# Kernel tuning notes

Hardware: AMD Instinct MI355X
Metric: run time of the kernel (lower is better)

Reference implementation:

```python
import jax, jax.numpy as jnp
import numpy as np

N_GAUSS, FEAT = 2048, 128
H, W = 128, 128
FX, FY = 128.0, 128.0
CX, CY = W / 2.0, H / 2.0
MAX_STEP = 0.05          # xyz_offset_max_step
CLIP_SCALING = 0.2       # clip_scaling
LOW_PASS = 0.3           # 2D covariance dilation (as in reference CUDA rasterizer)


def _quat_to_rot(q):
    # q: [N,4] normalized, (w,x,y,z) convention (rotation bias init has 1 at index 0)
    w, x, y, z = q[:, 0], q[:, 1], q[:, 2], q[:, 3]
    R = jnp.stack([
        1 - 2 * (y * y + z * z), 2 * (x * y - w * z), 2 * (x * z + w * y),
        2 * (x * y + w * z), 1 - 2 * (x * x + z * z), 2 * (y * z - w * x),
        2 * (x * z - w * y), 2 * (y * z + w * x), 1 - 2 * (x * x + y * y),
    ], axis=-1)
    return R.reshape(-1, 3, 3)


def setup_inputs() -> dict:
    key = jax.random.key(0)
    ks = jax.random.split(key, 8)
    s = 0.02
    x = jax.random.normal(ks[0], (N_GAUSS, FEAT), jnp.float32)
    pts = jax.random.normal(ks[1], (N_GAUSS, 3), jnp.float32) * 0.4
    # camera 2.5 units in front of the point cloud, looking down +z (view z = z + 2.5)
    viewmat = jnp.asarray(np.array(
        [[1, 0, 0, 0], [0, 1, 0, 0], [0, 0, 1, 2.5], [0, 0, 0, 1]], dtype=np.float32))
    w_shs = jax.random.normal(ks[2], (3, FEAT), jnp.float32) * s
    b_shs = jnp.zeros((3,), jnp.float32)
    w_scale = jax.random.normal(ks[3], (3, FEAT), jnp.float32) * s
    b_scale = jnp.full((3,), -3.0, jnp.float32)              # init_scaling
    w_xyz = jax.random.normal(ks[4], (3, FEAT), jnp.float32) * s
    b_xyz = jnp.zeros((3,), jnp.float32)
    w_opac = jax.random.normal(ks[5], (1, FEAT), jnp.float32) * s
    b_opac = jnp.full((1,), -2.1972246, jnp.float32)         # inverse_sigmoid(0.1)
    w_rot = jax.random.normal(ks[6], (4, FEAT), jnp.float32) * s
    b_rot = jnp.array([1.0, 0.0, 0.0, 0.0], jnp.float32)
    return dict(x=x, pts=pts, viewmat=viewmat, w_shs=w_shs, b_shs=b_shs,
                w_scale=w_scale, b_scale=b_scale, w_xyz=w_xyz, b_xyz=b_xyz,
                w_opac=w_opac, b_opac=b_opac, w_rot=w_rot, b_rot=b_rot)


def _forward(x, pts, viewmat, w_shs, b_shs, w_scale, b_scale, w_xyz, b_xyz,
             w_opac, b_opac, w_rot, b_rot):
    # ---- GSLayer decode (use_rgb=True path) ----
    rgb = jax.nn.sigmoid(x @ w_shs.T + b_shs)                     # [N,3]
    scale = jnp.clip(jnp.exp(x @ w_scale.T + b_scale), 0.0, CLIP_SCALING)
    offset = (jax.nn.sigmoid(x @ w_xyz.T + b_xyz) - 0.5) * MAX_STEP
    xyz = pts + offset                                            # [N,3]
    opac = jax.nn.sigmoid(x @ w_opac.T + b_opac)                  # [N,1]
    q = x @ w_rot.T + b_rot
    q = q / jnp.linalg.norm(q, axis=-1, keepdims=True)
    R = _quat_to_rot(q)                                           # [N,3,3]
    cov3d = jnp.einsum('nij,nj,nkj->nik', R, scale * scale, R)    # R S^2 R^T

    # ---- projection (EWA splatting) ----
    Rv, tv = viewmat[:3, :3], viewmat[:3, 3]
    p = xyz @ Rv.T + tv                                           # view space [N,3]
    tx, ty = p[:, 0], p[:, 1]
    tz = jnp.maximum(p[:, 2], 1e-3)
    u = FX * tx / tz + CX
    v = FY * ty / tz + CY
    zr = jnp.zeros_like(tz)
    J = jnp.stack([
        jnp.stack([FX / tz, zr, -FX * tx / (tz * tz)], axis=-1),
        jnp.stack([zr, FY / tz, -FY * ty / (tz * tz)], axis=-1),
    ], axis=1)                                                    # [N,2,3]
    M = jnp.einsum('nij,jk->nik', J, Rv)                          # [N,2,3]
    C2 = jnp.einsum('nij,njk,nlk->nil', M, cov3d, M)              # [N,2,2]
    a = C2[:, 0, 0] + LOW_PASS
    b = C2[:, 0, 1]
    c = C2[:, 1, 1] + LOW_PASS
    det = a * c - b * b + 1e-12
    cA, cB, cC = c / det, -b / det, a / det                       # conic

    # ---- per-pixel gaussian eval ----
    px = jnp.arange(W, dtype=jnp.float32) + 0.5
    py = jnp.arange(H, dtype=jnp.float32) + 0.5
    gx = jnp.tile(px, H)                                          # [P]
    gy = jnp.repeat(py, W)                                        # [P]
    dx = gx[None, :] - u[:, None]                                 # [N,P]
    dy = gy[None, :] - v[:, None]
    power = -0.5 * (cA[:, None] * dx * dx + cC[:, None] * dy * dy) - cB[:, None] * dx * dy
    power = jnp.minimum(power, 0.0)
    alpha = jnp.minimum(0.99, opac * jnp.exp(power))              # [N,P]
    vis = (p[:, 2] > 0.01).astype(alpha.dtype)[:, None]           # znear cull
    alpha = alpha * vis
    alpha = jnp.where(alpha < 1.0 / 255.0, 0.0, alpha)

    # ---- depth-sorted alpha compositing ----
    order = jnp.argsort(tz)
    alpha_s = alpha[order]
    rgb_s = rgb[order]
    T = jnp.cumprod(1.0 - alpha_s, axis=0)
    T_excl = jnp.concatenate([jnp.ones_like(T[:1]), T[:-1]], axis=0)
    wgt = alpha_s * T_excl                                        # [N,P]
    img = jnp.einsum('np,nc->pc', wgt, rgb_s).reshape(H, W, 3)
    return img


def reference(x, pts, viewmat, w_shs, b_shs, w_scale, b_scale, w_xyz, b_xyz,
              w_opac, b_opac, w_rot, b_rot):
    return _forward(x, pts, viewmat, w_shs, b_shs, w_scale, b_scale,
                    w_xyz, b_xyz, w_opac, b_opac, w_rot, b_rot)
```

## Files before the change

### kernel.cpp

```cpp
#include <hip/hip_runtime.h>
#include <math.h>

#define NG 2048
#define FEATN 128
#define NBLK 256
#define LOG2E 1.4426950408889634f
#define MAGIC1 0x7F3DC0DEu
#define MAGIC2 0x6B42F00Du

typedef unsigned long long u64;

#define RB_BYTE   32768
#define RC_BYTE   65536
#define KEY_BYTE  98304
#define SORT_BYTE 131072
#define F1_BYTE   229376
#define F2_BYTE   230400

__device__ __forceinline__ float sigmoidf_(float z) { return 1.0f / (1.0f + expf(-z)); }

__device__ __forceinline__ void stg8(void* p, u64 v) {
    __hip_atomic_store((u64*)p, v, __ATOMIC_RELAXED, __HIP_MEMORY_SCOPE_AGENT);
}
__device__ __forceinline__ void stg4(unsigned* p, unsigned v) {
    __hip_atomic_store(p, v, __ATOMIC_RELAXED, __HIP_MEMORY_SCOPE_AGENT);
}
__device__ __forceinline__ unsigned ldg4(const unsigned* p) {
    return __hip_atomic_load(p, __ATOMIC_RELAXED, __HIP_MEMORY_SCOPE_AGENT);
}
__device__ __forceinline__ void st_f4(void* p, float4 v) {
    union { float2 f; u64 u; } a, b;
    a.f = make_float2(v.x, v.y); b.f = make_float2(v.z, v.w);
    stg8(p, a.u); stg8((char*)p + 8, b.u);
}

__global__ __launch_bounds__(1024) void k_fused(
    const float* __restrict__ x, const float* __restrict__ pts, const float* __restrict__ vm,
    const float* __restrict__ w_shs, const float* __restrict__ b_shs,
    const float* __restrict__ w_scale, const float* __restrict__ b_scale,
    const float* __restrict__ w_xyz, const float* __restrict__ b_xyz,
    const float* __restrict__ w_opac, const float* __restrict__ b_opac,
    const float* __restrict__ w_rot, const float* __restrict__ b_rot,
    float* __restrict__ ws, float* __restrict__ out)
{
    __shared__ __attribute__((aligned(16))) char smem_u[512 * 12 * 4];
    __shared__ unsigned short sidx16[NG];
    __shared__ float partT[16][64], partR[16][64], partG[16][64], partB[16][64];
    __shared__ int s_cnt[16];
    __shared__ int s_break;

    float* sw = (float*)smem_u;
    float (*accs)[14] = (float(*)[14])(smem_u + 7168);
    unsigned* skey32 = (unsigned*)smem_u;
    float (*params_lds)[12] = (float(*)[12])smem_u;

    const int tid = threadIdx.x;
    const int wid = tid >> 6, lane = tid & 63;
    const int bid = blockIdx.x;
    char* wsb = (char*)ws;
    unsigned* keyg = (unsigned*)(wsb + KEY_BYTE);
    unsigned* flag1 = (unsigned*)(wsb + F1_BYTE);
    unsigned* flag2 = (unsigned*)(wsb + F2_BYTE);
    u64 lmask = (1ull << lane) - 1ull;

    for (int i = tid; i < 14 * FEATN; i += 1024) {
        int r = i >> 7, c0 = i & 127;
        float v;
        if (r < 3)       v = w_shs[r * FEATN + c0];
        else if (r < 6)  v = w_scale[(r - 3) * FEATN + c0];
        else if (r < 9)  v = w_xyz[(r - 6) * FEATN + c0];
        else if (r == 9) v = w_opac[c0];
        else             v = w_rot[(r - 10) * FEATN + c0];
        sw[i] = v;
    }
    __syncthreads();
    {
        int gi = tid >> 7;
        int head = (tid >> 3) & 15;
        int sub = tid & 7;
        int g = bid * 8 + gi;
        if (head < 14) {
            const float4* xp = (const float4*)(x + (size_t)g * FEATN + sub * 16);
            const float* wp = sw + head * FEATN + sub * 16;
            float acc = 0.0f;
#pragma unroll
            for (int k4 = 0; k4 < 4; k4++) {
                float4 xv = xp[k4];
                acc += xv.x * wp[k4 * 4 + 0] + xv.y * wp[k4 * 4 + 1]
                     + xv.z * wp[k4 * 4 + 2] + xv.w * wp[k4 * 4 + 3];
            }
            acc += __shfl_xor(acc, 1);
            acc += __shfl_xor(acc, 2);
            acc += __shfl_xor(acc, 4);
            if (sub == 0) accs[gi][head] = acc;
        }
    }
    __syncthreads();
    if (tid < 8) {
        int g = bid * 8 + tid;
        float acc[14];
#pragma unroll
        for (int j = 0; j < 14; j++) acc[j] = accs[tid][j];

        float r0 = sigmoidf_(acc[0] + b_shs[0]);
        float r1 = sigmoidf_(acc[1] + b_shs[1]);
        float r2 = sigmoidf_(acc[2] + b_shs[2]);
        float s0 = fminf(expf(acc[3] + b_scale[0]), 0.2f);
        float s1 = fminf(expf(acc[4] + b_scale[1]), 0.2f);
        float s2 = fminf(expf(acc[5] + b_scale[2]), 0.2f);
        float o0 = (sigmoidf_(acc[6] + b_xyz[0]) - 0.5f) * 0.05f;
        float o1 = (sigmoidf_(acc[7] + b_xyz[1]) - 0.5f) * 0.05f;
        float o2 = (sigmoidf_(acc[8] + b_xyz[2]) - 0.5f) * 0.05f;
        float opac = sigmoidf_(acc[9] + b_opac[0]);
        float qw = acc[10] + b_rot[0];
        float qx = acc[11] + b_rot[1];
        float qy = acc[12] + b_rot[2];
        float qz = acc[13] + b_rot[3];
        float qn = sqrtf(qw * qw + qx * qx + qy * qy + qz * qz);
        qw /= qn; qx /= qn; qy /= qn; qz /= qn;

        float R[3][3];
        R[0][0] = 1.f - 2.f * (qy * qy + qz * qz);
        R[0][1] = 2.f * (qx * qy - qw * qz);
        R[0][2] = 2.f * (qx * qz + qw * qy);
        R[1][0] = 2.f * (qx * qy + qw * qz);
        R[1][1] = 1.f - 2.f * (qx * qx + qz * qz);
        R[1][2] = 2.f * (qy * qz - qw * qx);
        R[2][0] = 2.f * (qx * qz - qw * qy);
        R[2][1] = 2.f * (qy * qz + qw * qx);
        R[2][2] = 1.f - 2.f * (qx * qx + qy * qy);

        float sq[3] = { s0 * s0, s1 * s1, s2 * s2 };
        float cov[3][3];
#pragma unroll
        for (int i = 0; i < 3; i++)
#pragma unroll
            for (int k = 0; k < 3; k++)
                cov[i][k] = R[i][0] * sq[0] * R[k][0] + R[i][1] * sq[1] * R[k][1] + R[i][2] * sq[2] * R[k][2];

        float Rv[3][3], tv[3];
#pragma unroll
        for (int i = 0; i < 3; i++) {
#pragma unroll
            for (int j = 0; j < 3; j++) Rv[i][j] = vm[i * 4 + j];
            tv[i] = vm[i * 4 + 3];
        }
        float X0 = pts[g * 3 + 0] + o0;
        float X1 = pts[g * 3 + 1] + o1;
        float X2 = pts[g * 3 + 2] + o2;
        float p0 = Rv[0][0] * X0 + Rv[0][1] * X1 + Rv[0][2] * X2 + tv[0];
        float p1 = Rv[1][0] * X0 + Rv[1][1] * X1 + Rv[1][2] * X2 + tv[1];
        float p2 = Rv[2][0] * X0 + Rv[2][1] * X1 + Rv[2][2] * X2 + tv[2];
        float tz = fmaxf(p2, 0.001f);
        float u = 128.0f * p0 / tz + 64.0f;
        float v = 128.0f * p1 / tz + 64.0f;

        float j00 = 128.0f / tz, j02 = -128.0f * p0 / (tz * tz);
        float j11 = 128.0f / tz, j12 = -128.0f * p1 / (tz * tz);
        float M0[3], M1[3];
#pragma unroll
        for (int k = 0; k < 3; k++) {
            M0[k] = j00 * Rv[0][k] + j02 * Rv[2][k];
            M1[k] = j11 * Rv[1][k] + j12 * Rv[2][k];
        }
        float t0[3], t1[3];
#pragma unroll
        for (int k = 0; k < 3; k++) {
            t0[k] = M0[0] * cov[0][k] + M0[1] * cov[1][k] + M0[2] * cov[2][k];
            t1[k] = M1[0] * cov[0][k] + M1[1] * cov[1][k] + M1[2] * cov[2][k];
        }
        float A = t0[0] * M0[0] + t0[1] * M0[1] + t0[2] * M0[2] + 0.3f;
        float B = t0[0] * M1[0] + t0[1] * M1[1] + t0[2] * M1[2];
        float C = t1[0] * M1[0] + t1[1] * M1[1] + t1[2] * M1[2] + 0.3f;
        float det = A * C - B * B + 1e-12f;
        float cA = C / det, cB = -B / det, cC = A / det;

        if (p2 <= 0.01f) opac = 0.0f;

        float rx, ry;
        if (opac >= 1.0f / 255.0f) {
            float L = 2.0f * logf(255.0f * opac);
            rx = sqrtf(L * A) + 0.5f;
            ry = sqrtf(L * C) + 0.5f;
        } else {
            rx = -1e9f; ry = -1e9f;
        }

        st_f4(wsb + (size_t)g * 16,            make_float4(u, v, rx, ry));
        st_f4(wsb + RB_BYTE + (size_t)g * 16,  make_float4(-0.5f * LOG2E * cA, -LOG2E * cB, -0.5f * LOG2E * cC, opac));
        st_f4(wsb + RC_BYTE + (size_t)g * 16,  make_float4(r0, r1, r2, 0.0f));
        stg4(&keyg[g], __float_as_uint(tz));
    }

    asm volatile("s_waitcnt vmcnt(0)" ::: "memory");
    __syncthreads();
    if (tid == 0) stg4(&flag1[bid], MAGIC1);
    if (tid < 256) {
        while (ldg4(&flag1[tid]) != MAGIC1) __builtin_amdgcn_s_sleep(4);
    }
    __syncthreads();

    ((u64*)skey32)[tid] = ((const u64*)keyg)[tid];
    __syncthreads();
    if (wid < 8) {
        int g = bid * 8 + wid;
        unsigned mk = skey32[g];
        const uint4* p4 = (const uint4*)skey32;
        int cnt = 0;
#pragma unroll
        for (int q = 0; q < 8; ++q) {
            int jb = lane + (q << 6);
            uint4 kv = p4[jb];
            int j0 = jb << 2;
            cnt += (kv.x < mk || (kv.x == mk && (j0 + 0) < g)) ? 1 : 0;
            cnt += (kv.y < mk || (kv.y == mk && (j0 + 1) < g)) ? 1 : 0;
            cnt += (kv.z < mk || (kv.z == mk && (j0 + 2) < g)) ? 1 : 0;
            cnt += (kv.w < mk || (kv.w == mk && (j0 + 3) < g)) ? 1 : 0;
        }
        cnt += __shfl_xor(cnt, 1);
        cnt += __shfl_xor(cnt, 2);
        cnt += __shfl_xor(cnt, 4);
        cnt += __shfl_xor(cnt, 8);
        cnt += __shfl_xor(cnt, 16);
        cnt += __shfl_xor(cnt, 32);
        if (lane < 6) {
            const u64* src = (const u64*)(wsb + (lane >> 1) * 32768 + (size_t)g * 16 + (lane & 1) * 8);
            char* dst = wsb + SORT_BYTE + (lane >> 1) * 32768 + (size_t)cnt * 16 + (lane & 1) * 8;
            stg8(dst, *src);
        }
    }

    asm volatile("s_waitcnt vmcnt(0)" ::: "memory");
    __syncthreads();
    if (tid == 0) stg4(&flag2[bid], MAGIC2);
    if (tid < 256) {
        while (ldg4(&flag2[tid]) != MAGIC2) __builtin_amdgcn_s_sleep(4);
    }
    __syncthreads();

    const float4* SA4 = (const float4*)(wsb + SORT_BYTE);
    const float4* SB4 = (const float4*)(wsb + SORT_BYTE + 32768);
    const float4* SC4 = (const float4*)(wsb + SORT_BYTE + 65536);
    int tx0 = (bid & 15) << 3, ty0 = (bid >> 4) << 3;
    float x0 = tx0 + 0.5f, x1 = tx0 + 7.5f;
    float y0 = ty0 + 0.5f, y1 = ty0 + 7.5f;

    int n = 0;
#pragma unroll
    for (int r = 0; r < 2; ++r) {
        int s = r * 1024 + tid;
        float4 a = SA4[s];
        bool keep = (a.x + a.z >= x0) && (a.x - a.z <= x1) &&
                    (a.y + a.w >= y0) && (a.y - a.w <= y1);
        u64 m = __ballot(keep);
        if (lane == 0) s_cnt[wid] = __popcll(m);
        __syncthreads();
        int base = n, total = 0;
#pragma unroll
        for (int w = 0; w < 16; w++) {
            if (w < wid) base += s_cnt[w];
            total += s_cnt[w];
        }
        if (keep) sidx16[base + __popcll(m & lmask)] = (unsigned short)s;
        n += total;
        __syncthreads();
    }

    float gx = x0 + (float)(lane & 7);
    float gy = y0 + (float)(lane >> 3);
    float crT = 1.0f, crR = 0.0f, crG = 0.0f, crB = 0.0f;
    for (int c0 = 0; c0 < n; c0 += 512) {
        int m = min(512, n - c0);
        if (tid < m) {
            int s = sidx16[c0 + tid];
            float4 a = SA4[s];
            float4 b = SB4[s];
            float4 c = SC4[s];
            float* e = params_lds[tid];
            ((float4*)e)[0] = make_float4(a.x, a.y, b.x, b.y);
            ((float4*)e)[1] = make_float4(b.z, b.w, c.x, c.y);
            e[8] = c.z;
        }
        __syncthreads();

        int seg = (m + 15) >> 4;
        int sb = wid * seg;
        int se = min(m, sb + seg);
        float T = 1.0f, oR = 0.0f, oG = 0.0f, oB = 0.0f;
        for (int i = sb; i < se; ++i) {
            const float* e = params_lds[i];
            float4 e0 = ((const float4*)e)[0];
            float4 e1 = ((const float4*)e)[1];
            float bl = e[8];
            float dx = gx - e0.x, dy = gy - e0.y;
            float pw = dx * (e0.z * dx + e0.w * dy) + e1.x * dy * dy;
            pw = fminf(pw, 0.0f);
            float al = fminf(0.99f, e1.y * exp2f(pw));
            al = (al < 1.0f / 255.0f) ? 0.0f : al;
            float w = al * T;
            oR += w * e1.z;
            oG += w * e1.w;
            oB += w * bl;
            T -= al * T;
        }
        partT[wid][lane] = T;
        partR[wid][lane] = oR;
        partG[wid][lane] = oG;
        partB[wid][lane] = oB;
        __syncthreads();

        if (wid == 0) {
#pragma unroll
            for (int w = 0; w < 16; w++) {
                crR += crT * partR[w][lane];
                crG += crT * partG[w][lane];
                crB += crT * partB[w][lane];
                crT *= partT[w][lane];
            }
            u64 alive = __ballot(crT >= 1.5e-5f);
            if (lane == 0) s_break = (alive == 0ull);
        }
        __syncthreads();
        if (s_break) break;
    }

    if (wid == 0) {
        int p = (ty0 + (lane >> 3)) * 128 + tx0 + (lane & 7);
        out[p * 3 + 0] = crR;
        out[p * 3 + 1] = crG;
        out[p * 3 + 2] = crB;
    }
}

extern "C" void kernel_launch(void* const* d_in, const int* in_sizes, int n_in,
                              void* d_out, int out_size, void* d_ws, size_t ws_size,
                              hipStream_t stream)
{
    const float* x       = (const float*)d_in[0];
    const float* pts     = (const float*)d_in[1];
    const float* viewmat = (const float*)d_in[2];
    const float* w_shs   = (const float*)d_in[3];
    const float* b_shs   = (const float*)d_in[4];
    const float* w_scale = (const float*)d_in[5];
    const float* b_scale = (const float*)d_in[6];
    const float* w_xyz   = (const float*)d_in[7];
    const float* b_xyz   = (const float*)d_in[8];
    const float* w_opac  = (const float*)d_in[9];
    const float* b_opac  = (const float*)d_in[10];
    const float* w_rot   = (const float*)d_in[11];
    const float* b_rot   = (const float*)d_in[12];
    float* ws = (float*)d_ws;
    float* out = (float*)d_out;

    k_fused<<<NBLK, 1024, 0, stream>>>(x, pts, viewmat, w_shs, b_shs, w_scale, b_scale,
                                       w_xyz, b_xyz, w_opac, b_opac, w_rot, b_rot, ws, out);
}
```

Baseline: 25.50 us.

## Pack gaussian params into fp16 cull records and 32-byte bf16 render records

Shrinks the per-gaussian workspace layout. Culling now reads a compact fp16 (u,v,rx,ry) record, and the render parameters are packed into two float4s with R and G stored as bf16. This lets the LDS chunk grow from 512 to 1024 entries with 8-float records, so fewer chunk iterations and barriers are needed. The weight staging through LDS is dropped in favour of direct global reads, and the cull loop is merged into a single pass. The fp16 bounding radii (padded to 0.6) and bf16 colours add small precision loss in exchange for less memory traffic.

```diff
diff --git a/kernel.cpp b/kernel.cpp
--- a/kernel.cpp
+++ b/kernel.cpp
@@ -1,4 +1,5 @@
 #include <hip/hip_runtime.h>
+#include <hip/hip_fp16.h>
 #include <math.h>
 
 #define NG 2048
@@ -10,12 +11,14 @@
 
 typedef unsigned long long u64;
 
-#define RB_BYTE   32768
-#define RC_BYTE   65536
-#define KEY_BYTE  98304
-#define SORT_BYTE 131072
-#define F1_BYTE   229376
-#define F2_BYTE   230400
+#define RAW1_B 16384
+#define RAW2_B 49152
+#define KEY_B  81920
+#define S0_B   98304
+#define S1_B   131072
+#define S2_B   163840
+#define F1_B   229376
+#define F2_B   230400
 
 __device__ __forceinline__ float sigmoidf_(float z) { return 1.0f / (1.0f + expf(-z)); }
 
@@ -32,6 +35,10 @@
     union { float2 f; u64 u; } a, b;
     a.f = make_float2(v.x, v.y); b.f = make_float2(v.z, v.w);
     stg8(p, a.u); stg8((char*)p + 8, b.u);
+}
+__device__ __forceinline__ unsigned short bf16_(float f) {
+    unsigned u = __float_as_uint(f);
+    return (unsigned short)((u + 0x8000u) >> 16);
 }
 
 __global__ __launch_bounds__(1024) void k_fused(
@@ -43,45 +50,39 @@
     const float* __restrict__ w_rot, const float* __restrict__ b_rot,
     float* __restrict__ ws, float* __restrict__ out)
 {
-    __shared__ __attribute__((aligned(16))) char smem_u[512 * 12 * 4];
+    __shared__ __attribute__((aligned(16))) char smem_u[1024 * 8 * 4];
     __shared__ unsigned short sidx16[NG];
     __shared__ float partT[16][64], partR[16][64], partG[16][64], partB[16][64];
-    __shared__ int s_cnt[16];
+    __shared__ int s_cnt0[16], s_cnt1[16];
     __shared__ int s_break;
 
-    float* sw = (float*)smem_u;
-    float (*accs)[14] = (float(*)[14])(smem_u + 7168);
+    float (*accs)[14] = (float(*)[14])smem_u;
     unsigned* skey32 = (unsigned*)smem_u;
-    float (*params_lds)[12] = (float(*)[12])smem_u;
+    float* params_lds = (float*)smem_u;
 
     const int tid = threadIdx.x;
     const int wid = tid >> 6, lane = tid & 63;
     const int bid = blockIdx.x;
     char* wsb = (char*)ws;
-    unsigned* keyg = (unsigned*)(wsb + KEY_BYTE);
-    unsigned* flag1 = (unsigned*)(wsb + F1_BYTE);
-    unsigned* flag2 = (unsigned*)(wsb + F2_BYTE);
+    unsigned* keyg = (unsigned*)(wsb + KEY_B);
+    unsigned* flag1 = (unsigned*)(wsb + F1_B);
+    unsigned* flag2 = (unsigned*)(wsb + F2_B);
     u64 lmask = (1ull << lane) - 1ull;
 
-    for (int i = tid; i < 14 * FEATN; i += 1024) {
-        int r = i >> 7, c0 = i & 127;
-        float v;
-        if (r < 3)       v = w_shs[r * FEATN + c0];
-        else if (r < 6)  v = w_scale[(r - 3) * FEATN + c0];
-        else if (r < 9)  v = w_xyz[(r - 6) * FEATN + c0];
-        else if (r == 9) v = w_opac[c0];
-        else             v = w_rot[(r - 10) * FEATN + c0];
-        sw[i] = v;
-    }
-    __syncthreads();
     {
         int gi = tid >> 7;
         int head = (tid >> 3) & 15;
         int sub = tid & 7;
         int g = bid * 8 + gi;
         if (head < 14) {
+            const float* wbase;
+            if (head < 3)       wbase = w_shs + head * FEATN;
+            else if (head < 6)  wbase = w_scale + (head - 3) * FEATN;
+            else if (head < 9)  wbase = w_xyz + (head - 6) * FEATN;
+            else if (head == 9) wbase = w_opac;
+            else                wbase = w_rot + (head - 10) * FEATN;
             const float4* xp = (const float4*)(x + (size_t)g * FEATN + sub * 16);
-            const float* wp = sw + head * FEATN + sub * 16;
+            const float* wp = wbase + sub * 16;
             float acc = 0.0f;
 #pragma unroll
             for (int k4 = 0; k4 < 4; k4++) {
@@ -180,15 +181,22 @@
         float rx, ry;
         if (opac >= 1.0f / 255.0f) {
             float L = 2.0f * logf(255.0f * opac);
-            rx = sqrtf(L * A) + 0.5f;
-            ry = sqrtf(L * C) + 0.5f;
+            rx = sqrtf(L * A) + 0.6f;
+            ry = sqrtf(L * C) + 0.6f;
         } else {
             rx = -1e9f; ry = -1e9f;
         }
 
-        st_f4(wsb + (size_t)g * 16,            make_float4(u, v, rx, ry));
-        st_f4(wsb + RB_BYTE + (size_t)g * 16,  make_float4(-0.5f * LOG2E * cA, -LOG2E * cB, -0.5f * LOG2E * cC, opac));
-        st_f4(wsb + RC_BYTE + (size_t)g * 16,  make_float4(r0, r1, r2, 0.0f));
+        u64 h0 = (u64)__half_as_ushort(__float2half(u))
+               | ((u64)__half_as_ushort(__float2half(v)) << 16)
+               | ((u64)__half_as_ushort(__float2half(rx)) << 32)
+               | ((u64)__half_as_ushort(__float2half(ry)) << 48);
+        stg8(wsb + (size_t)g * 8, h0);
+        st_f4(wsb + RAW1_B + (size_t)g * 16,
+              make_float4(u, v, -0.5f * LOG2E * cA, -LOG2E * cB));
+        unsigned rg = (unsigned)bf16_(r0) | ((unsigned)bf16_(r1) << 16);
+        st_f4(wsb + RAW2_B + (size_t)g * 16,
+              make_float4(-0.5f * LOG2E * cC, opac, __uint_as_float(rg), r2));
         stg4(&keyg[g], __float_as_uint(tz));
     }
 
@@ -223,10 +231,17 @@
         cnt += __shfl_xor(cnt, 8);
         cnt += __shfl_xor(cnt, 16);
         cnt += __shfl_xor(cnt, 32);
-        if (lane < 6) {
-            const u64* src = (const u64*)(wsb + (lane >> 1) * 32768 + (size_t)g * 16 + (lane & 1) * 8);
-            char* dst = wsb + SORT_BYTE + (lane >> 1) * 32768 + (size_t)cnt * 16 + (lane & 1) * 8;
-            stg8(dst, *src);
+        if (lane < 5) {
+            u64 v; char* dst;
+            if (lane == 0) {
+                v = *(const u64*)(wsb + (size_t)g * 8);
+                dst = wsb + S0_B + (size_t)cnt * 8;
+            } else {
+                int ai = (lane - 1) >> 1, hf = (lane - 1) & 1;
+                v = *(const u64*)(wsb + (ai ? RAW2_B : RAW1_B) + (size_t)g * 16 + hf * 8);
+                dst = wsb + (ai ? S2_B : S1_B) + (size_t)cnt * 16 + hf * 8;
+            }
+            stg8(dst, v);
         }
     }
 
@@ -238,48 +253,54 @@
     }
     __syncthreads();
 
-    const float4* SA4 = (const float4*)(wsb + SORT_BYTE);
-    const float4* SB4 = (const float4*)(wsb + SORT_BYTE + 32768);
-    const float4* SC4 = (const float4*)(wsb + SORT_BYTE + 65536);
+    const u64* S0_64 = (const u64*)(wsb + S0_B);
+    const float4* S1_4 = (const float4*)(wsb + S1_B);
+    const float4* S2_4 = (const float4*)(wsb + S2_B);
     int tx0 = (bid & 15) << 3, ty0 = (bid >> 4) << 3;
     float x0 = tx0 + 0.5f, x1 = tx0 + 7.5f;
     float y0 = ty0 + 0.5f, y1 = ty0 + 7.5f;
 
-    int n = 0;
-#pragma unroll
-    for (int r = 0; r < 2; ++r) {
-        int s = r * 1024 + tid;
-        float4 a = SA4[s];
-        bool keep = (a.x + a.z >= x0) && (a.x - a.z <= x1) &&
-                    (a.y + a.w >= y0) && (a.y - a.w <= y1);
-        u64 m = __ballot(keep);
-        if (lane == 0) s_cnt[wid] = __popcll(m);
-        __syncthreads();
-        int base = n, total = 0;
+    int n;
+    {
+        int sA = tid, sB = tid + 1024;
+        u64 pa = S0_64[sA], pb = S0_64[sB];
+        float ua = __half2float(__ushort_as_half((unsigned short)pa));
+        float va = __half2float(__ushort_as_half((unsigned short)(pa >> 16)));
+        float ra = __half2float(__ushort_as_half((unsigned short)(pa >> 32)));
+        float ya = __half2float(__ushort_as_half((unsigned short)(pa >> 48)));
+        float ub = __half2float(__ushort_as_half((unsigned short)pb));
+        float vb = __half2float(__ushort_as_half((unsigned short)(pb >> 16)));
+        float rb = __half2float(__ushort_as_half((unsigned short)(pb >> 32)));
+        float yb = __half2float(__ushort_as_half((unsigned short)(pb >> 48)));
+        bool kA = (ua + ra >= x0) && (ua - ra <= x1) && (va + ya >= y0) && (va - ya <= y1);
+        bool kB = (ub + rb >= x0) && (ub - rb <= x1) && (vb + yb >= y0) && (vb - yb <= y1);
+        u64 m0 = __ballot(kA), m1 = __ballot(kB);
+        if (lane == 0) { s_cnt0[wid] = __popcll(m0); s_cnt1[wid] = __popcll(m1); }
+        __syncthreads();
+        int b0 = 0, t0 = 0, b1 = 0, t1 = 0;
 #pragma unroll
         for (int w = 0; w < 16; w++) {
-            if (w < wid) base += s_cnt[w];
-            total += s_cnt[w];
-        }
-        if (keep) sidx16[base + __popcll(m & lmask)] = (unsigned short)s;
-        n += total;
+            if (w < wid) { b0 += s_cnt0[w]; b1 += s_cnt1[w]; }
+            t0 += s_cnt0[w]; t1 += s_cnt1[w];
+        }
+        if (kA) sidx16[b0 + __popcll(m0 & lmask)] = (unsigned short)sA;
+        if (kB) sidx16[t0 + b1 + __popcll(m1 & lmask)] = (unsigned short)sB;
+        n = t0 + t1;
         __syncthreads();
     }
 
     float gx = x0 + (float)(lane & 7);
     float gy = y0 + (float)(lane >> 3);
     float crT = 1.0f, crR = 0.0f, crG = 0.0f, crB = 0.0f;
-    for (int c0 = 0; c0 < n; c0 += 512) {
-        int m = min(512, n - c0);
+    for (int c0 = 0; c0 < n; c0 += 1024) {
+        int m = min(1024, n - c0);
         if (tid < m) {
             int s = sidx16[c0 + tid];
-            float4 a = SA4[s];
-            float4 b = SB4[s];
-            float4 c = SC4[s];
-            float* e = params_lds[tid];
-            ((float4*)e)[0] = make_float4(a.x, a.y, b.x, b.y);
-            ((float4*)e)[1] = make_float4(b.z, b.w, c.x, c.y);
-            e[8] = c.z;
+            float4 a = S1_4[s];
+            float4 b = S2_4[s];
+            float4* e = (float4*)(params_lds + tid * 8);
+            e[0] = a;
+            e[1] = b;
         }
         __syncthreads();
 
@@ -288,19 +309,19 @@
         int se = min(m, sb + seg);
         float T = 1.0f, oR = 0.0f, oG = 0.0f, oB = 0.0f;
         for (int i = sb; i < se; ++i) {
-            const float* e = params_lds[i];
-            float4 e0 = ((const float4*)e)[0];
-            float4 e1 = ((const float4*)e)[1];
-            float bl = e[8];
+            const float4* e = (const float4*)(params_lds + i * 8);
+            float4 e0 = e[0];
+            float4 e1 = e[1];
             float dx = gx - e0.x, dy = gy - e0.y;
             float pw = dx * (e0.z * dx + e0.w * dy) + e1.x * dy * dy;
             pw = fminf(pw, 0.0f);
             float al = fminf(0.99f, e1.y * exp2f(pw));
             al = (al < 1.0f / 255.0f) ? 0.0f : al;
             float w = al * T;
-            oR += w * e1.z;
-            oG += w * e1.w;
-            oB += w * bl;
+            unsigned rgb = __float_as_uint(e1.z);
+            oR += w * __uint_as_float(rgb << 16);
+            oG += w * __uint_as_float(rgb & 0xffff0000u);
+            oB += w * e1.w;
             T -= al * T;
         }
         partT[wid][lane] = T;
```

Measured after the change: 25.76 us. About the same (+1.1%).
